# Optimization experiments

Measured on AMD Instinct MI355X. Metric: run time of the kernel, lower is better.

Reference implementation:

```python
import jax, jax.numpy as jnp
import numpy as np

SMOOTHING = 0.1
EPSILON = 1e-08


def setup_inputs() -> dict:
    key = jax.random.key(0)
    k1, k2 = jax.random.split(key)
    B, S, C = 2, 2048, 32000
    outputs = jax.random.normal(k1, (B, S, C), dtype=jnp.float32)
    gold_label_ids = jax.random.randint(k2, (B, S), 0, C, dtype=jnp.int64)
    mask = jnp.ones((B, S), dtype=bool)
    weight = jnp.ones((C,), dtype=jnp.float32)
    return {"outputs": outputs, "gold_label_ids": gold_label_ids, "mask": mask, "weight": weight}


def reference(outputs, gold_label_ids, mask, weight):
    B, S, C = outputs.shape
    N = B * S
    logits = outputs.reshape(N, C)
    gold = gold_label_ids.reshape(N)

    nll = -jax.nn.log_softmax(logits, axis=-1)  # [N, C]

    # Label-smoothed target: uniform = s/(C-1) everywhere, confidence at gold.
    # loss_i = sum_c w_c * nll_ic * smooth_ic
    #        = uniform * sum_c(w_c * nll_ic) + (confidence - uniform) * w_g * nll_ig
    uniform = SMOOTHING / (C - 1)
    confidence = 1.0 - SMOOTHING
    total = jnp.einsum('nc,c->n', nll, weight)  # sum of weighted nll per row
    gold_nll = jnp.take_along_axis(nll, gold[:, None], axis=1)[:, 0]
    gold_w = weight[gold]
    loss = uniform * total + (confidence - uniform) * gold_w * gold_nll  # [N]

    seq_mask = mask.reshape(N).astype(loss.dtype)
    loss = loss * seq_mask
    return jnp.sum(loss) / (jnp.sum(seq_mask) + EPSILON)
```

## Files before the change

kernel.cpp:

```cpp
#include <hip/hip_runtime.h>
#include <math.h>

#define SMOOTHING 0.1f
#define EPSILON_F 1e-8f
#define LOG2E_F   1.44269504088896340736f
#define DEFER_THR 10.0f

typedef float vf4 __attribute__((ext_vector_type(4)));

__device__ __forceinline__ float fexp2(float x) { return __builtin_amdgcn_exp2f(x); }

__device__ __forceinline__ vf4 ntload4(const vf4* p) {
    return __builtin_nontemporal_load(p);
}

__device__ __forceinline__ void osm_combine(float& m, float& s, float mo, float so) {
    float nm = fmaxf(m, mo);
    s = s * fexp2((m - nm) * LOG2E_F) + so * fexp2((mo - nm) * LOG2E_F);
    m = nm;
}

__device__ __forceinline__ void osm_update4(float& M, float& nMs, float& S,
                                            vf4 v, vf4 w, float& wd, float& ws) {
    float c01 = fmaxf(v.x, v.y);
    float c23 = fmaxf(v.z, v.w);
    float cm  = fmaxf(c01, c23);
    if (__builtin_expect(cm > M + DEFER_THR, 0)) {
        S *= fexp2((M - cm) * LOG2E_F);
        M = cm;
        nMs = -M * LOG2E_F;
    }
    float e0 = fexp2(fmaf(v.x, LOG2E_F, nMs));
    float e1 = fexp2(fmaf(v.y, LOG2E_F, nMs));
    float e2 = fexp2(fmaf(v.z, LOG2E_F, nMs));
    float e3 = fexp2(fmaf(v.w, LOG2E_F, nMs));
    S += (e0 + e1) + (e2 + e3);
    wd = fmaf(w.x, v.x, wd);
    wd = fmaf(w.y, v.y, wd);
    wd = fmaf(w.z, v.z, wd);
    wd = fmaf(w.w, v.w, wd);
    ws += (w.x + w.y) + (w.z + w.w);
}

__global__ __launch_bounds__(256) void Seq2SeqLoss_row_kernel(
    const float* __restrict__ logits,
    const int*   __restrict__ gold,
    const int*   __restrict__ mask,
    const float* __restrict__ weight,
    float*       __restrict__ row_loss,
    int C)
{
    const int row = blockIdx.x;
    const int tid = threadIdx.x;
    const float* __restrict__ x = logits + (size_t)row * (size_t)C;

    const int   g  = gold[row];
    const int   mk = mask[row];
    const float xg = x[g];
    const float wg = weight[g];

    const int C4   = C >> 2;
    const int half = C4 >> 1;
    const vf4* __restrict__ x4  = (const vf4*)x;
    const vf4* __restrict__ x4h = x4 + half;
    const vf4* __restrict__ w4  = (const vf4*)weight;
    const vf4* __restrict__ w4h = w4 + half;

    float M0 = -1e30f, nMs0 = 0.f, S0 = 0.f;
    float M1 = -1e30f, nMs1 = 0.f, S1 = 0.f;
    float wd = 0.f, wsum = 0.f;

    for (int i = tid; i < half; i += 256) {
        vf4 a  = ntload4(x4  + i);
        vf4 b  = ntload4(x4h + i);
        vf4 wa = w4[i];
        vf4 wb = w4h[i];
        osm_update4(M0, nMs0, S0, a, wa, wd, wsum);
        osm_update4(M1, nMs1, S1, b, wb, wd, wsum);
    }
    for (int i = (half << 1) + tid; i < C4; i += 256) {
        vf4 a  = ntload4(x4 + i);
        vf4 wa = w4[i];
        osm_update4(M0, nMs0, S0, a, wa, wd, wsum);
    }

    osm_combine(M0, S0, M1, S1);
    float M = M0, S = S0;

    #pragma unroll
    for (int off = 32; off >= 1; off >>= 1) {
        float Mo = __shfl_down(M, off);
        float So = __shfl_down(S, off);
        wd   += __shfl_down(wd, off);
        wsum += __shfl_down(wsum, off);
        osm_combine(M, S, Mo, So);
    }

    __shared__ float shM[4], shS[4], shWD[4], shWS[4];
    const int wave = tid >> 6;
    if ((tid & 63) == 0) { shM[wave] = M; shS[wave] = S; shWD[wave] = wd; shWS[wave] = wsum; }
    __syncthreads();

    if (tid == 0) {
        #pragma unroll
        for (int w = 1; w < 4; ++w) {
            osm_combine(M, S, shM[w], shS[w]);
            wd   += shWD[w];
            wsum += shWS[w];
        }
        float logZ = M + logf(S);

        const float uniform    = SMOOTHING / (float)(C - 1);
        const float confidence = 1.0f - SMOOTHING;

        float total    = logZ * wsum - wd;
        float gold_nll = logZ - xg;
        float loss = uniform * total + (confidence - uniform) * wg * gold_nll;

        loss *= (mk != 0) ? 1.0f : 0.0f;
        row_loss[row] = loss;
    }
}

__global__ __launch_bounds__(1024) void Seq2SeqLoss_finalize_kernel(
    const float* __restrict__ row_loss,
    const int*   __restrict__ mask,
    float*       __restrict__ out,
    int N)
{
    const int tid = threadIdx.x;
    float acc = 0.f, cnt = 0.f;
    for (int i = tid; i < N; i += 1024) {
        acc += row_loss[i];
        cnt += (mask[i] != 0) ? 1.0f : 0.0f;
    }
    #pragma unroll
    for (int off = 32; off >= 1; off >>= 1) {
        acc += __shfl_down(acc, off);
        cnt += __shfl_down(cnt, off);
    }
    __shared__ float shA[16], shC[16];
    const int wave = tid >> 6;
    if ((tid & 63) == 0) { shA[wave] = acc; shC[wave] = cnt; }
    __syncthreads();
    if (tid == 0) {
        #pragma unroll
        for (int w = 1; w < 16; ++w) { acc += shA[w]; cnt += shC[w]; }
        out[0] = acc / (cnt + EPSILON_F);
    }
}

extern "C" void kernel_launch(void* const* d_in, const int* in_sizes, int n_in,
                              void* d_out, int out_size, void* d_ws, size_t ws_size,
                              hipStream_t stream) {
    const float* logits = (const float*)d_in[0];
    const int*   gold   = (const int*)d_in[1];
    const int*   mask   = (const int*)d_in[2];
    const float* weight = (const float*)d_in[3];

    const int N = in_sizes[1];
    const int C = in_sizes[3];

    float* row_loss = (float*)d_ws;

    Seq2SeqLoss_row_kernel<<<N, 256, 0, stream>>>(logits, gold, mask, weight, row_loss, C);
    Seq2SeqLoss_finalize_kernel<<<1, 1024, 0, stream>>>(row_loss, mask, (float*)d_out, N);
}
```

Measured before the change: 643.5 us.

## Prefetch next tile in row loop and hoist weight-sum into finalize kernel

Each row block no longer computes the sum of all class weights. It writes per-row partials (logZ, weighted dot, gold term, mask), and the finalize kernel computes the weight sum once and assembles the loss. The main loop is also software-pipelined, loading the next iteration's logits and weights into registers before processing the current ones, to hide memory latency. This costs extra registers and a slightly larger workspace write per row.

After: 648.4 us. About the same (+0.8%).

```diff
diff --git a/kernel.cpp b/kernel.cpp
--- a/kernel.cpp
+++ b/kernel.cpp
@@ -21,10 +21,8 @@
 }
 
 __device__ __forceinline__ void osm_update4(float& M, float& nMs, float& S,
-                                            vf4 v, vf4 w, float& wd, float& ws) {
-    float c01 = fmaxf(v.x, v.y);
-    float c23 = fmaxf(v.z, v.w);
-    float cm  = fmaxf(c01, c23);
+                                            vf4 v, vf4 w, float& wd) {
+    float cm = fmaxf(fmaxf(v.x, v.y), fmaxf(v.z, v.w));
     if (__builtin_expect(cm > M + DEFER_THR, 0)) {
         S *= fexp2((M - cm) * LOG2E_F);
         M = cm;
@@ -39,7 +37,6 @@
     wd = fmaf(w.y, v.y, wd);
     wd = fmaf(w.z, v.z, wd);
     wd = fmaf(w.w, v.w, wd);
-    ws += (w.x + w.y) + (w.z + w.w);
 }
 
 __global__ __launch_bounds__(256) void Seq2SeqLoss_row_kernel(
@@ -47,7 +44,7 @@
     const int*   __restrict__ gold,
     const int*   __restrict__ mask,
     const float* __restrict__ weight,
-    float*       __restrict__ row_loss,
+    vf4*         __restrict__ row_part,
     int C)
 {
     const int row = blockIdx.x;
@@ -68,20 +65,31 @@
 
     float M0 = -1e30f, nMs0 = 0.f, S0 = 0.f;
     float M1 = -1e30f, nMs1 = 0.f, S1 = 0.f;
-    float wd = 0.f, wsum = 0.f;
+    float wd = 0.f;
 
+    vf4 a, b, wa, wb;
+    {
+        int ic = (tid < half) ? tid : 0;
+        a  = ntload4(x4  + ic);
+        b  = ntload4(x4h + ic);
+        wa = w4[ic];
+        wb = w4h[ic];
+    }
     for (int i = tid; i < half; i += 256) {
-        vf4 a  = ntload4(x4  + i);
-        vf4 b  = ntload4(x4h + i);
-        vf4 wa = w4[i];
-        vf4 wb = w4h[i];
-        osm_update4(M0, nMs0, S0, a, wa, wd, wsum);
-        osm_update4(M1, nMs1, S1, b, wb, wd, wsum);
+        int j  = i + 256;
+        int jc = (j < half) ? j : i;
+        vf4 a2  = ntload4(x4  + jc);
+        vf4 b2  = ntload4(x4h + jc);
+        vf4 wa2 = w4[jc];
+        vf4 wb2 = w4h[jc];
+        osm_update4(M0, nMs0, S0, a, wa, wd);
+        osm_update4(M1, nMs1, S1, b, wb, wd);
+        a = a2; b = b2; wa = wa2; wb = wb2;
     }
     for (int i = (half << 1) + tid; i < C4; i += 256) {
-        vf4 a  = ntload4(x4 + i);
-        vf4 wa = w4[i];
-        osm_update4(M0, nMs0, S0, a, wa, wd, wsum);
+        vf4 va = ((const vf4*)x)[i];
+        vf4 vw = w4[i];
+        osm_update4(M0, nMs0, S0, va, vw, wd);
     }
 
     osm_combine(M0, S0, M1, S1);
@@ -91,56 +99,78 @@
     for (int off = 32; off >= 1; off >>= 1) {
         float Mo = __shfl_down(M, off);
         float So = __shfl_down(S, off);
-        wd   += __shfl_down(wd, off);
-        wsum += __shfl_down(wsum, off);
+        wd += __shfl_down(wd, off);
         osm_combine(M, S, Mo, So);
     }
 
-    __shared__ float shM[4], shS[4], shWD[4], shWS[4];
+    __shared__ float shM[4], shS[4], shWD[4];
     const int wave = tid >> 6;
-    if ((tid & 63) == 0) { shM[wave] = M; shS[wave] = S; shWD[wave] = wd; shWS[wave] = wsum; }
+    if ((tid & 63) == 0) { shM[wave] = M; shS[wave] = S; shWD[wave] = wd; }
     __syncthreads();
 
     if (tid == 0) {
         #pragma unroll
         for (int w = 1; w < 4; ++w) {
             osm_combine(M, S, shM[w], shS[w]);
-            wd   += shWD[w];
-            wsum += shWS[w];
+            wd += shWD[w];
         }
         float logZ = M + logf(S);
-
-        const float uniform    = SMOOTHING / (float)(C - 1);
-        const float confidence = 1.0f - SMOOTHING;
-
-        float total    = logZ * wsum - wd;
-        float gold_nll = logZ - xg;
-        float loss = uniform * total + (confidence - uniform) * wg * gold_nll;
-
-        loss *= (mk != 0) ? 1.0f : 0.0f;
-        row_loss[row] = loss;
+        vf4 out;
+        out.x = logZ;
+        out.y = wd;
+        out.z = wg * (logZ - xg);
+        out.w = (mk != 0) ? 1.0f : 0.0f;
+        row_part[row] = out;
     }
 }
 
 __global__ __launch_bounds__(1024) void Seq2SeqLoss_finalize_kernel(
-    const float* __restrict__ row_loss,
-    const int*   __restrict__ mask,
+    const vf4*   __restrict__ row_part,
+    const float* __restrict__ weight,
     float*       __restrict__ out,
-    int N)
+    int N, int C)
 {
-    const int tid = threadIdx.x;
+    const int tid  = threadIdx.x;
+    const int wave = tid >> 6;
+    __shared__ float shA[16], shC[16], shW[16], shBroadcast;
+
+    float ws = 0.f;
+    const int C4 = C >> 2;
+    const vf4* w4 = (const vf4*)weight;
+    for (int i = tid; i < C4; i += 1024) {
+        vf4 w = w4[i];
+        ws += (w.x + w.y) + (w.z + w.w);
+    }
+    for (int i = (C4 << 2) + tid; i < C; i += 1024) ws += weight[i];
+    #pragma unroll
+    for (int off = 32; off >= 1; off >>= 1) ws += __shfl_down(ws, off);
+    if ((tid & 63) == 0) shW[wave] = ws;
+    __syncthreads();
+    if (tid == 0) {
+        float t = 0.f;
+        #pragma unroll
+        for (int w = 0; w < 16; ++w) t += shW[w];
+        shBroadcast = t;
+    }
+    __syncthreads();
+    const float wsum = shBroadcast;
+
+    const float uniform    = SMOOTHING / (float)(C - 1);
+    const float confidence = 1.0f - SMOOTHING;
+    const float kgold      = confidence - uniform;
+
     float acc = 0.f, cnt = 0.f;
     for (int i = tid; i < N; i += 1024) {
-        acc += row_loss[i];
-        cnt += (mask[i] != 0) ? 1.0f : 0.0f;
+        vf4 p = row_part[i];
+        float loss = uniform * fmaf(p.x, wsum, -p.y) + kgold * p.z;
+        acc += p.w * loss;
+        cnt += p.w;
     }
     #pragma unroll
     for (int off = 32; off >= 1; off >>= 1) {
         acc += __shfl_down(acc, off);
         cnt += __shfl_down(cnt, off);
     }
-    __shared__ float shA[16], shC[16];
-    const int wave = tid >> 6;
     if ((tid & 63) == 0) { shA[wave] = acc; shC[wave] = cnt; }
     __syncthreads();
     if (tid == 0) {
@@ -161,8 +191,8 @@
     const int N = in_sizes[1];
     const int C = in_sizes[3];
 
-    float* row_loss = (float*)d_ws;
+    vf4* row_part = (vf4*)d_ws;
 
-    Seq2SeqLoss_row_kernel<<<N, 256, 0, stream>>>(logits, gold, mask, weight, row_loss, C);
-    Seq2SeqLoss_finalize_kernel<<<1, 1024, 0, stream>>>(row_loss, mask, (float*)d_out, N);
+    Seq2SeqLoss_row_kernel<<<N, 256, 0, stream>>>(logits, gold, mask, weight, row_part, C);
+    Seq2SeqLoss_finalize_kernel<<<1, 1024, 0, stream>>>(row_part, weight, (float*)d_out, N, C);
 }
```
